# Optimization experiments

Measured on AMD Instinct MI355X. Metric: run time of the kernel, lower is better.

Reference implementation:

```python
import jax, jax.numpy as jnp
import numpy as np

N_NODES = 50000
N_EDGES = 800000
D_FEAT = 128
HIDDEN = 128
OUT = 64
HEADS = 4


def setup_inputs() -> dict:
    key = jax.random.key(0)
    ks = jax.random.split(key, 12)
    s_in = 1.0 / np.sqrt(D_FEAT)
    s_h = 1.0 / np.sqrt(HIDDEN)
    x = jax.random.normal(ks[0], (N_NODES, D_FEAT), dtype=jnp.float32)
    edge_index = jax.random.randint(ks[1], (2, N_EDGES), 0, N_NODES, dtype=jnp.int32)
    return {
        "x": x,
        "edge_index": edge_index,
        # SAGEConv params: lin_l (aggregated neighbors), lin_r (root), bias
        "W_l": jax.random.normal(ks[2], (D_FEAT, HIDDEN), dtype=jnp.float32) * s_in,
        "W_r": jax.random.normal(ks[3], (D_FEAT, HIDDEN), dtype=jnp.float32) * s_in,
        "b_sage": jnp.zeros((HIDDEN,), dtype=jnp.float32),
        # GATConv params: lin_src, lin_dst (heads*hidden each), att vectors, bias
        "W_src": jax.random.normal(ks[4], (HIDDEN, HEADS * HIDDEN), dtype=jnp.float32) * s_h,
        "W_dst": jax.random.normal(ks[5], (HIDDEN, HEADS * HIDDEN), dtype=jnp.float32) * s_h,
        "att_src": jax.random.normal(ks[6], (HEADS, HIDDEN), dtype=jnp.float32) * s_h,
        "att_dst": jax.random.normal(ks[7], (HEADS, HIDDEN), dtype=jnp.float32) * s_h,
        "b_gat": jnp.zeros((HIDDEN,), dtype=jnp.float32),
        # Final Linear
        "W_lin": jax.random.normal(ks[8], (HIDDEN, OUT), dtype=jnp.float32) * s_h,
        "b_lin": jnp.zeros((OUT,), dtype=jnp.float32),
    }


def reference(x, edge_index, W_l, W_r, b_sage, W_src, W_dst, att_src, att_dst, b_gat, W_lin, b_lin):
    N = x.shape[0]
    src = edge_index[0]
    dst = edge_index[1]

    # ---- SAGEConv (mean aggregation): out = lin_l(mean_j x_j) + lin_r(x_i) + b ----
    agg = jax.ops.segment_sum(x[src], dst, num_segments=N)          # [N, d]
    cnt = jax.ops.segment_sum(jnp.ones_like(dst, dtype=x.dtype), dst, num_segments=N)
    mean_nbr = agg / jnp.maximum(cnt, 1.0)[:, None]
    h = mean_nbr @ W_l + x @ W_r + b_sage                           # [N, H*... no: [N, hidden]
    h = jax.nn.relu(h)

    # ---- GATConv (heads=4, concat=False -> mean over heads) ----
    H, C = att_src.shape
    hs = (h @ W_src).reshape(N, H, C)                               # source-transformed [N, H, C]
    hd = (h @ W_dst).reshape(N, H, C)                               # dest-transformed   [N, H, C]
    a_s = jnp.einsum('nhc,hc->nh', hs, att_src)                     # [N, H]
    a_d = jnp.einsum('nhc,hc->nh', hd, att_dst)                     # [N, H]
    e = jax.nn.leaky_relu(a_s[src] + a_d[dst], negative_slope=0.2)  # [E, H]
    # edge softmax over incoming edges per destination node
    e_max = jax.ops.segment_max(e, dst, num_segments=N)             # [N, H]
    e_exp = jnp.exp(e - e_max[dst])                                 # [E, H]
    denom = jax.ops.segment_sum(e_exp, dst, num_segments=N)         # [N, H]
    alpha = e_exp / denom[dst]                                      # [E, H]
    msg = hs[src] * alpha[:, :, None]                               # [E, H, C]
    out = jax.ops.segment_sum(msg, dst, num_segments=N)             # [N, H, C]
    out = out.mean(axis=1) + b_gat                                  # concat=False: avg heads
    out = jax.nn.relu(out)

    # ---- final Linear ----
    return out @ W_lin + b_lin
```

## Files before the change

kernel.cpp:

```cpp
#include <hip/hip_runtime.h>

#define D 128
#define HEADS 4

typedef __attribute__((ext_vector_type(8))) short short8;
typedef __attribute__((ext_vector_type(4))) float f32x4;

static __device__ __forceinline__ float leaky(float v) { return v > 0.f ? v : 0.2f * v; }

static __device__ __forceinline__ float2 bf2_to_f2(unsigned int u) {
    float2 r;
    union { unsigned int i; float f; } a, b;
    a.i = (u & 0xffffu) << 16;
    b.i = u & 0xffff0000u;
    r.x = a.f; r.y = b.f;
    return r;
}
static __device__ __forceinline__ float bf_to_f(unsigned short s) {
    union { unsigned int i; float f; } a;
    a.i = ((unsigned int)s) << 16;
    return a.f;
}
static __device__ __forceinline__ unsigned short f2bf(float f) {
    union { float f; unsigned int i; } v; v.f = f;
    unsigned int u = v.i;
    unsigned int r = (u + 0x7fffu + ((u >> 16) & 1u)) >> 16;
    return (unsigned short)r;
}

#define CPAD 16
#define HIST_BLOCKS 128
#define PREP_CNT 107520

__global__ __launch_bounds__(256) void k_early(const float* __restrict__ x,
                                               const int* __restrict__ ei, int E, int npairs,
                                               const float* __restrict__ Wl, const float* __restrict__ Wr,
                                               const float* __restrict__ Wsrc, const float* __restrict__ Wlin,
                                               const float* __restrict__ Wdst,
                                               const float* __restrict__ atts, const float* __restrict__ attd,
                                               unsigned short* __restrict__ Bh,
                                               unsigned short* __restrict__ Bg,
                                               unsigned short* __restrict__ Bf,
                                               float* __restrict__ wsd,
                                               unsigned int* __restrict__ xb,
                                               int* __restrict__ bhist) {
    __shared__ int sh[512];
    int gb = blockIdx.x, t = threadIdx.x;
    if (gb < HIST_BLOCKS) {
        for (int i = t; i < 512; i += 256) sh[i] = 0;
        __syncthreads();
        for (int i = gb * 256 + t; i < E; i += HIST_BLOCKS * 256)
            atomicAdd(&sh[ei[E + i] >> 7], 1);
        __syncthreads();
        for (int i = t; i < 512; i += 256) if (sh[i]) atomicAdd(&bhist[i * CPAD], sh[i]);
        return;
    }
    int i = (gb - HIST_BLOCKS) * 256 + t;
    if (i < 32768) {
        int idx = i;
        int j = idx & 7, n16 = (idx >> 3) & 15, quad = (idx >> 7) & 3, rest = idx >> 9;
        int nc = rest & 7, kb = rest >> 3;
        int kk = kb * 32 + quad * 8 + j;
        int n = nc * 16 + n16;
        float v = (kk < 128) ? Wl[kk * 128 + n] : Wr[(kk - 128) * 128 + n];
        Bh[idx] = f2bf(v);
    } else if (i < 32768 + 65536) {
        int idx = i - 32768;
        int j = idx & 7, n16 = (idx >> 3) & 15, quad = (idx >> 7) & 3, rest = idx >> 9;
        int nc = rest & 7, kb = rest >> 3;
        int kk = kb * 32 + quad * 8 + j;
        int n = nc * 16 + n16;
        float v = Wsrc[(kk & 127) * 512 + (kk >> 7) * 128 + n];
        Bg[idx] = f2bf(v);
    } else if (i < 32768 + 65536 + 8192) {
        int idx = i - 98304;
        int j = idx & 7, n16 = (idx >> 3) & 15, quad = (idx >> 7) & 3, rest = idx >> 9;
        int nc = rest & 3, kb = rest >> 2;
        int kk = kb * 32 + quad * 8 + j;
        int n = nc * 16 + n16;
        Bf[idx] = f2bf(Wlin[kk * 64 + n]);
    } else if (i < PREP_CNT) {
        int tt = i - 106496;
        int k = tt >> 3, o = tt & 7;
        int hh = o & 3;
        const float* W = (o < 4) ? Wsrc : Wdst;
        const float* att = (o < 4) ? atts : attd;
        float acc = 0.f;
        for (int c = 0; c < 128; c++) acc += W[k * 512 + hh * 128 + c] * att[hh * 128 + c];
        wsd[k * 8 + o] = acc;
    } else {
        int p = i - PREP_CNT;
        if (p < npairs) {
            float2 v = *(const float2*)(x + (size_t)p * 2);
            xb[p] = (unsigned int)f2bf(v.x) | ((unsigned int)f2bf(v.y) << 16);
        }
    }
}

__global__ void k_bscan(const int* __restrict__ bhist, int nbuck, int E,
                        int* __restrict__ bbase, int* __restrict__ bcur,
                        int* __restrict__ rowptr, int N) {
    __shared__ int s[512];
    int t = threadIdx.x;
    int v = (t < nbuck) ? bhist[t * CPAD] : 0;
    s[t] = v;
    __syncthreads();
    for (int off = 1; off < 512; off <<= 1) {
        int tv = (t >= off) ? s[t - off] : 0;
        __syncthreads();
        s[t] += tv;
        __syncthreads();
    }
    if (t < nbuck) { int ex = s[t] - v; bbase[t] = ex; bcur[t * CPAD] = ex; }
    if (t == 0) { bbase[nbuck] = E; rowptr[N] = E; }
}

__global__ __launch_bounds__(256) void k_binscatter(const int* __restrict__ ei, int E,
                                                    int* __restrict__ bcur,
                                                    int2* __restrict__ ebuf) {
    int i = blockIdx.x * 256 + threadIdx.x;
    if (i < E) {
        int s = ei[i], d = ei[E + i];
        int pos = atomicAdd(&bcur[(d >> 7) * CPAD], 1);
        ebuf[pos] = make_int2(s, d);
    }
}

__global__ __launch_bounds__(256) void k_bucket_csr(const int2* __restrict__ ebuf,
                                                    const int* __restrict__ bbase,
                                                    int2* __restrict__ csr2,
                                                    int* __restrict__ rowptr, int N) {
    __shared__ int cnt[128];
    __shared__ int incl[128];
    __shared__ unsigned char off[4608];
    __shared__ int2 sorted[4608];
    int b = blockIdx.x;
    int e0 = bbase[b], e1 = bbase[b + 1];
    int ecnt = e1 - e0;
    if (ecnt > 4608) ecnt = 4608;
    int t = threadIdx.x;
    if (t < 128) cnt[t] = 0;
    __syncthreads();
    for (int i = t; i < ecnt; i += 256) {
        int d = ebuf[e0 + i].y & 127;
        off[i] = (unsigned char)atomicAdd(&cnt[d], 1);
    }
    __syncthreads();
    if (t < 128) incl[t] = cnt[t];
    __syncthreads();
    for (int o = 1; o < 128; o <<= 1) {
        int v = 0;
        if (t < 128 && t >= o) v = incl[t - o];
        __syncthreads();
        if (t < 128) incl[t] += v;
        __syncthreads();
    }
    int nbase0 = b << 7;
    if (t < 128) {
        int node = nbase0 + t;
        if (node < N) rowptr[node] = e0 + incl[t] - cnt[t];
    }
    __syncthreads();
    for (int i = t; i < ecnt; i += 256) {
        int2 e = ebuf[e0 + i];
        int d = e.y & 127;
        sorted[incl[d] - cnt[d] + off[i]] = e;
    }
    __syncthreads();
    for (int i = t; i < ecnt; i += 256) csr2[e0 + i] = sorted[i];
}

__global__ __launch_bounds__(256) void k_sage_mean(const int* __restrict__ rowptr,
                                                   const int2* __restrict__ csr2,
                                                   const unsigned int* __restrict__ xb,
                                                   unsigned int* __restrict__ meanb, int N) {
    int n = blockIdx.x * 4 + (threadIdx.x >> 6);
    if (n >= N) return;
    int lane = threadIdx.x & 63;
    int e0 = rowptr[n], e1 = rowptr[n + 1];
    float ax = 0.f, ay = 0.f;
    int e = e0;
    for (; e + 3 < e1; e += 4) {
        int s0 = csr2[e].x, s1 = csr2[e + 1].x, s2 = csr2[e + 2].x, s3 = csr2[e + 3].x;
        unsigned int u0 = xb[(size_t)s0 * 64 + lane];
        unsigned int u1 = xb[(size_t)s1 * 64 + lane];
        unsigned int u2 = xb[(size_t)s2 * 64 + lane];
        unsigned int u3 = xb[(size_t)s3 * 64 + lane];
        float2 v0 = bf2_to_f2(u0), v1 = bf2_to_f2(u1), v2 = bf2_to_f2(u2), v3 = bf2_to_f2(u3);
        ax += (v0.x + v1.x) + (v2.x + v3.x);
        ay += (v0.y + v1.y) + (v2.y + v3.y);
    }
    for (; e < e1; e++) {
        int s0 = csr2[e].x;
        float2 v0 = bf2_to_f2(xb[(size_t)s0 * 64 + lane]);
        ax += v0.x; ay += v0.y;
    }
    int dg = e1 - e0;
    float inv = 1.0f / (float)(dg > 0 ? dg : 1);
    unsigned int o = (unsigned int)f2bf(ax * inv) | ((unsigned int)f2bf(ay * inv) << 16);
    __builtin_nontemporal_store(o, meanb + (size_t)n * 64 + lane);
}

__global__ __launch_bounds__(256) void k_mfma_h(const unsigned short* __restrict__ A0,
                                                const unsigned short* __restrict__ A1,
                                                const unsigned short* __restrict__ Bp,
                                                const float* __restrict__ bias,
                                                const float* __restrict__ wsd,
                                                unsigned short* __restrict__ outb,
                                                float* __restrict__ a_s,
                                                float* __restrict__ a_d, int M) {
    const int NC = 8;
    __shared__ unsigned short sH[64][136];
    __shared__ float swsd[1024];
    int tid = threadIdx.x;
    int wave = tid >> 6;
    int lane = tid & 63;
    int row0 = blockIdx.x * 64 + wave * 16;
    int n16 = lane & 15, quad = lane >> 4;
    int arow = row0 + n16;
    int arowc = arow < M ? arow : 0;
    for (int i = tid; i < 1024; i += 256) swsd[i] = wsd[i];
    f32x4 acc[NC];
    #pragma unroll
    for (int i = 0; i < NC; i++) acc[i] = (f32x4){0.f, 0.f, 0.f, 0.f};
    #pragma unroll
    for (int kb = 0; kb < 8; kb++) {
        const unsigned short* ap = (kb < 4)
            ? (A0 + (size_t)arowc * 128 + kb * 32 + quad * 8)
            : (A1 + (size_t)arowc * 128 + (kb - 4) * 32 + quad * 8);
        short8 af = *(const short8*)ap;
        #pragma unroll
        for (int nc = 0; nc < NC; nc++) {
            short8 bf = *(const short8*)(Bp + ((((size_t)(kb * NC + nc) * 4 + quad) * 16 + n16) << 3));
            acc[nc] = __builtin_amdgcn_mfma_f32_16x16x32_bf16(af, bf, acc[nc], 0, 0, 0);
        }
    }
    int orow = row0 + quad * 4;
    int lrow = wave * 16 + quad * 4;
    #pragma unroll
    for (int r = 0; r < 4; r++) {
        int m = orow + r;
        #pragma unroll
        for (int nc = 0; nc < NC; nc++) {
            int col = nc * 16 + n16;
            float v = fmaxf(acc[nc][r] + bias[col], 0.f);
            unsigned short bv = f2bf(v);
            sH[lrow + r][col] = bv;
            if (m < M) outb[(size_t)m * 128 + col] = bv;
        }
    }
    __syncthreads();
    #pragma unroll
    for (int j = tid; j < 512; j += 256) {
        int m = j >> 3, o = j & 7;
        float accd = 0.f;
        #pragma unroll 4
        for (int k = 0; k < 128; k++)
            accd += bf_to_f(sH[m][k]) * swsd[k * 8 + o];
        int n = blockIdx.x * 64 + m;
        if (n < M) {
            if (o < 4) a_s[n * 4 + o] = accd;
            else       a_d[n * 4 + (o - 4)] = accd;
        }
    }
}

#define EDGE_CAP 192
__global__ __launch_bounds__(256) void k_gat_agg(const int* __restrict__ rowptr,
                                                 const int2* __restrict__ csr2,
                                                 const unsigned int* __restrict__ hb,
                                                 const float* __restrict__ a_s,
                                                 const float* __restrict__ a_d,
                                                 unsigned int* __restrict__ aggb, int N) {
    __shared__ int   sSrc[4][EDGE_CAP];
    __shared__ float sAl[4][EDGE_CAP * 4];
    int wv = threadIdx.x >> 6;
    int lane = threadIdx.x & 63;
    int n = blockIdx.x * 4 + wv;
    bool active = n < N;
    int e0 = 0, deg = 0;
    float4 ad = {0.f, 0.f, 0.f, 0.f};
    if (active) {
        e0 = rowptr[n];
        deg = rowptr[n + 1] - e0;
        ad = *(const float4*)(a_d + (size_t)n * 4);
    }
    f32x4 psum = {0.f, 0.f, 0.f, 0.f};
    for (int base = 0; base < deg; base += 64) {
        int i = base + lane;
        if (i < deg) {
            int s = csr2[e0 + i].x;
            float4 as = *(const float4*)(a_s + (size_t)s * 4);
            f32x4 w;
            w.x = __expf(leaky(as.x + ad.x));
            w.y = __expf(leaky(as.y + ad.y));
            w.z = __expf(leaky(as.z + ad.z));
            w.w = __expf(leaky(as.w + ad.w));
            psum += w;
            if (i < EDGE_CAP) {
                sSrc[wv][i] = s;
                *(f32x4*)&sAl[wv][i * 4] = w;
            }
        }
    }
    #pragma unroll
    for (int o = 32; o; o >>= 1) {
        psum.x += __shfl_xor(psum.x, o);
        psum.y += __shfl_xor(psum.y, o);
        psum.z += __shfl_xor(psum.z, o);
        psum.w += __shfl_xor(psum.w, o);
    }
    f32x4 inv;
    inv.x = psum.x > 0.f ? 0.25f / psum.x : 0.f;
    inv.y = psum.y > 0.f ? 0.25f / psum.y : 0.f;
    inv.z = psum.z > 0.f ? 0.25f / psum.z : 0.f;
    inv.w = psum.w > 0.f ? 0.25f / psum.w : 0.f;
    int capdeg = deg < EDGE_CAP ? deg : EDGE_CAP;
    for (int base = 0; base < capdeg; base += 64) {
        int i = base + lane;
        if (i < capdeg) {
            f32x4 w = *(f32x4*)&sAl[wv][i * 4];
            w *= inv;
            *(f32x4*)&sAl[wv][i * 4] = w;
        }
    }
    __syncthreads();
    float2 ac0 = {0, 0}, ac1 = {0, 0}, ac2 = {0, 0}, ac3 = {0, 0};
    int e = 0;
    for (; e + 3 < capdeg; e += 4) {
        int s0 = sSrc[wv][e], s1 = sSrc[wv][e + 1], s2 = sSrc[wv][e + 2], s3 = sSrc[wv][e + 3];
        f32x4 w0 = *(const f32x4*)&sAl[wv][e * 4];
        f32x4 w1 = *(const f32x4*)&sAl[wv][e * 4 + 4];
        f32x4 w2 = *(const f32x4*)&sAl[wv][e * 4 + 8];
        f32x4 w3 = *(const f32x4*)&sAl[wv][e * 4 + 12];
        unsigned int u0 = hb[(size_t)s0 * 64 + lane];
        unsigned int u1 = hb[(size_t)s1 * 64 + lane];
        unsigned int u2 = hb[(size_t)s2 * 64 + lane];
        unsigned int u3 = hb[(size_t)s3 * 64 + lane];
        float2 v0 = bf2_to_f2(u0), v1 = bf2_to_f2(u1), v2 = bf2_to_f2(u2), v3 = bf2_to_f2(u3);
        ac0.x += w0.x * v0.x + w1.x * v1.x + w2.x * v2.x + w3.x * v3.x;
        ac0.y += w0.x * v0.y + w1.x * v1.y + w2.x * v2.y + w3.x * v3.y;
        ac1.x += w0.y * v0.x + w1.y * v1.x + w2.y * v2.x + w3.y * v3.x;
        ac1.y += w0.y * v0.y + w1.y * v1.y + w2.y * v2.y + w3.y * v3.y;
        ac2.x += w0.z * v0.x + w1.z * v1.x + w2.z * v2.x + w3.z * v3.x;
        ac2.y += w0.z * v0.y + w1.z * v1.y + w2.z * v2.y + w3.z * v3.y;
        ac3.x += w0.w * v0.x + w1.w * v1.x + w2.w * v2.x + w3.w * v3.x;
        ac3.y += w0.w * v0.y + w1.w * v1.y + w2.w * v2.y + w3.w * v3.y;
    }
    for (; e < capdeg; e++) {
        int s0 = sSrc[wv][e];
        f32x4 w0 = *(const f32x4*)&sAl[wv][e * 4];
        unsigned int u0 = hb[(size_t)s0 * 64 + lane];
        float2 v0 = bf2_to_f2(u0);
        ac0.x += w0.x * v0.x; ac0.y += w0.x * v0.y;
        ac1.x += w0.y * v0.x; ac1.y += w0.y * v0.y;
        ac2.x += w0.z * v0.x; ac2.y += w0.z * v0.y;
        ac3.x += w0.w * v0.x; ac3.y += w0.w * v0.y;
    }
    for (int i = EDGE_CAP; i < deg; i++) {
        int s = csr2[e0 + i].x;
        float4 as = *(const float4*)(a_s + (size_t)s * 4);
        f32x4 w;
        w.x = __expf(leaky(as.x + ad.x)) * inv.x;
        w.y = __expf(leaky(as.y + ad.y)) * inv.y;
        w.z = __expf(leaky(as.z + ad.z)) * inv.z;
        w.w = __expf(leaky(as.w + ad.w)) * inv.w;
        float2 v0 = bf2_to_f2(hb[(size_t)s * 64 + lane]);
        ac0.x += w.x * v0.x; ac0.y += w.x * v0.y;
        ac1.x += w.y * v0.x; ac1.y += w.y * v0.y;
        ac2.x += w.z * v0.x; ac2.y += w.z * v0.y;
        ac3.x += w.w * v0.x; ac3.y += w.w * v0.y;
    }
    if (!active) return;
    unsigned int* rowu = aggb + (size_t)n * 256 + lane;
    unsigned int o0 = (unsigned int)f2bf(ac0.x) | ((unsigned int)f2bf(ac0.y) << 16);
    unsigned int o1 = (unsigned int)f2bf(ac1.x) | ((unsigned int)f2bf(ac1.y) << 16);
    unsigned int o2 = (unsigned int)f2bf(ac2.x) | ((unsigned int)f2bf(ac2.y) << 16);
    unsigned int o3 = (unsigned int)f2bf(ac3.x) | ((unsigned int)f2bf(ac3.y) << 16);
    __builtin_nontemporal_store(o0, rowu + 0);
    __builtin_nontemporal_store(o1, rowu + 64);
    __builtin_nontemporal_store(o2, rowu + 128);
    __builtin_nontemporal_store(o3, rowu + 192);
}

__global__ __launch_bounds__(256) void k_mfma_tail(const unsigned short* __restrict__ aggb,
                                                   const unsigned short* __restrict__ Bg,
                                                   const float* __restrict__ bg,
                                                   const unsigned short* __restrict__ Bf,
                                                   const float* __restrict__ bl,
                                                   float* __restrict__ out, int M) {
    __shared__ unsigned short sG[64][136];
    int wave = threadIdx.x >> 6;
    int lane = threadIdx.x & 63;
    int row0 = blockIdx.x * 64 + wave * 16;
    int n16 = lane & 15, quad = lane >> 4;
    {
        int arow = row0 + n16;
        int arowc = arow < M ? arow : 0;
        const unsigned short* ap = aggb + (size_t)arowc * 512 + quad * 8;
        f32x4 acc[8];
        #pragma unroll
        for (int i = 0; i < 8; i++) acc[i] = (f32x4){0.f, 0.f, 0.f, 0.f};
        #pragma unroll
        for (int kb = 0; kb < 16; kb++) {
            short8 af = *(const short8*)(ap + kb * 32);
            #pragma unroll
            for (int nc = 0; nc < 8; nc++) {
                short8 bf = *(const short8*)(Bg + ((((size_t)(kb * 8 + nc) * 4 + quad) * 16 + n16) << 3));
                acc[nc] = __builtin_amdgcn_mfma_f32_16x16x32_bf16(af, bf, acc[nc], 0, 0, 0);
            }
        }
        int lrow = wave * 16 + quad * 4;
        #pragma unroll
        for (int r = 0; r < 4; r++) {
            #pragma unroll
            for (int nc = 0; nc < 8; nc++) {
                int col = nc * 16 + n16;
                sG[lrow + r][col] = f2bf(fmaxf(acc[nc][r] + bg[col], 0.f));
            }
        }
    }
    __syncthreads();
    {
        f32x4 acc[4];
        #pragma unroll
        for (int i = 0; i < 4; i++) acc[i] = (f32x4){0.f, 0.f, 0.f, 0.f};
        #pragma unroll
        for (int kb = 0; kb < 4; kb++) {
            short8 af = *(const short8*)&sG[wave * 16 + n16][kb * 32 + quad * 8];
            #pragma unroll
            for (int nc = 0; nc < 4; nc++) {
                short8 bf = *(const short8*)(Bf + ((((size_t)(kb * 4 + nc) * 4 + quad) * 16 + n16) << 3));
                acc[nc] = __builtin_amdgcn_mfma_f32_16x16x32_bf16(af, bf, acc[nc], 0, 0, 0);
            }
        }
        int orow = row0 + quad * 4;
        #pragma unroll
        for (int r = 0; r < 4; r++) {
            int m = orow + r;
            if (m < M) {
                #pragma unroll
                for (int nc = 0; nc < 4; nc++) {
                    int col = nc * 16 + n16;
                    out[(size_t)m * 64 + col] = acc[nc][r] + bl[col];
                }
            }
        }
    }
}

extern "C" void kernel_launch(void* const* d_in, const int* in_sizes, int n_in,
                              void* d_out, int out_size, void* d_ws, size_t ws_size,
                              hipStream_t stream) {
    const float* x    = (const float*)d_in[0];
    const int*   ei   = (const int*)d_in[1];
    const float* Wl   = (const float*)d_in[2];
    const float* Wr   = (const float*)d_in[3];
    const float* bs   = (const float*)d_in[4];
    const float* Wsrc = (const float*)d_in[5];
    const float* Wdst = (const float*)d_in[6];
    const float* atts = (const float*)d_in[7];
    const float* attd = (const float*)d_in[8];
    const float* bg   = (const float*)d_in[9];
    const float* Wlin = (const float*)d_in[10];
    const float* bl   = (const float*)d_in[11];
    int N = in_sizes[0] / D;
    int E = in_sizes[1] / 2;
    int nbuck = (N + 127) >> 7;
    int npairs = N * 64;

    char* w = (char*)d_ws;
    auto alloc = [&](size_t bytes) {
        char* p = w;
        w += (bytes + 255) & ~(size_t)255;
        return p;
    };
    unsigned int* xb     = (unsigned int*)alloc((size_t)N * 256);
    unsigned int* meanb  = (unsigned int*)alloc((size_t)N * 256);
    unsigned int* hb     = (unsigned int*)alloc((size_t)N * 256);
    unsigned int* aggb   = (unsigned int*)alloc((size_t)N * 1024);
    unsigned short* Bh   = (unsigned short*)alloc(65536 * 2);
    unsigned short* Bg   = (unsigned short*)alloc(65536 * 2);
    unsigned short* Bf   = (unsigned short*)alloc(8192 * 2);
    float* a_s           = (float*)alloc((size_t)N * 16);
    float* a_d           = (float*)alloc((size_t)N * 16);
    float* wsd           = (float*)alloc(1024 * 4);
    int* rowptr          = (int*)alloc((size_t)(N + 512) * 4);
    int* bhist           = (int*)alloc(512 * CPAD * 4);
    int* bbase           = (int*)alloc(513 * 4);
    int* bcur            = (int*)alloc(512 * CPAD * 4);
    int2* ebuf           = (int2*)alloc((size_t)E * 8);
    int2* csr2           = (int2*)alloc((size_t)E * 8);
    (void)ws_size; (void)n_in; (void)out_size;

    hipMemsetAsync(bhist, 0, 512 * CPAD * 4, stream);

    int workBlocks = (PREP_CNT + npairs + 255) / 256;
    k_early<<<HIST_BLOCKS + workBlocks, 256, 0, stream>>>(x, ei, E, npairs,
                                                          Wl, Wr, Wsrc, Wlin, Wdst, atts, attd,
                                                          Bh, Bg, Bf, wsd, xb, bhist);
    k_bscan<<<1, 512, 0, stream>>>(bhist, nbuck, E, bbase, bcur, rowptr, N);
    k_binscatter<<<(E + 255) / 256, 256, 0, stream>>>(ei, E, bcur, ebuf);
    k_bucket_csr<<<nbuck, 256, 0, stream>>>(ebuf, bbase, csr2, rowptr, N);

    k_sage_mean<<<(N + 3) / 4, 256, 0, stream>>>(rowptr, csr2, xb, meanb, N);
    k_mfma_h<<<(N + 63) / 64, 256, 0, stream>>>((const unsigned short*)meanb,
                                                (const unsigned short*)xb, Bh, bs, wsd,
                                                (unsigned short*)hb, a_s, a_d, N);
    k_gat_agg<<<(N + 3) / 4, 256, 0, stream>>>(rowptr, csr2, hb, a_s, a_d, aggb, N);
    k_mfma_tail<<<(N + 63) / 64, 256, 0, stream>>>((const unsigned short*)aggb, Bg, bg,
                                                   Bf, bl, (float*)d_out, N);
}
```

Measured before the change: 294.4 us.

## Fuse CSR bucket sort with SAGE mean aggregation using 32-node buckets

Shrinks destination buckets from 128 to 32 nodes and packs each edge into one 32-bit word (16-bit source plus 5-bit local destination). A new kernel sorts each bucket in shared memory and immediately computes the SAGE neighbour means from the sorted sources, replacing the separate CSR-build and mean kernels. The CSR also drops from int2 to int, which halves edge-index traffic in the GAT aggregation. The trade-offs are that the 16-bit packing only holds for fewer than 65536 nodes, each bucket is capped at 1024 edges, and each wave now processes 8 nodes serially.

```diff
diff --git a/kernel.cpp b/kernel.cpp
--- a/kernel.cpp
+++ b/kernel.cpp
@@ -31,6 +31,7 @@
 #define CPAD 16
 #define HIST_BLOCKS 128
 #define PREP_CNT 107520
+#define MAXBUCK 2048
 
 __global__ __launch_bounds__(256) void k_early(const float* __restrict__ x,
                                                const int* __restrict__ ei, int E, int npairs,
@@ -44,15 +45,15 @@
                                                float* __restrict__ wsd,
                                                unsigned int* __restrict__ xb,
                                                int* __restrict__ bhist) {
-    __shared__ int sh[512];
+    __shared__ int sh[MAXBUCK];
     int gb = blockIdx.x, t = threadIdx.x;
     if (gb < HIST_BLOCKS) {
-        for (int i = t; i < 512; i += 256) sh[i] = 0;
+        for (int i = t; i < MAXBUCK; i += 256) sh[i] = 0;
         __syncthreads();
         for (int i = gb * 256 + t; i < E; i += HIST_BLOCKS * 256)
-            atomicAdd(&sh[ei[E + i] >> 7], 1);
+            atomicAdd(&sh[ei[E + i] >> 5], 1);
         __syncthreads();
-        for (int i = t; i < 512; i += 256) if (sh[i]) atomicAdd(&bhist[i * CPAD], sh[i]);
+        for (int i = t; i < MAXBUCK; i += 256) if (sh[i]) atomicAdd(&bhist[i * CPAD], sh[i]);
         return;
     }
     int i = (gb - HIST_BLOCKS) * 256 + t;
@@ -97,108 +98,115 @@
     }
 }
 
-__global__ void k_bscan(const int* __restrict__ bhist, int nbuck, int E,
-                        int* __restrict__ bbase, int* __restrict__ bcur,
-                        int* __restrict__ rowptr, int N) {
-    __shared__ int s[512];
+__global__ __launch_bounds__(256) void k_bscan(const int* __restrict__ bhist, int nbuck, int E,
+                                               int* __restrict__ bbase, int* __restrict__ bcur,
+                                               int* __restrict__ rowptr, int N) {
+    __shared__ int ssum[256];
     int t = threadIdx.x;
-    int v = (t < nbuck) ? bhist[t * CPAD] : 0;
-    s[t] = v;
-    __syncthreads();
-    for (int off = 1; off < 512; off <<= 1) {
-        int tv = (t >= off) ? s[t - off] : 0;
+    int base = t * 8;
+    int v[8]; int s = 0;
+    #pragma unroll
+    for (int j = 0; j < 8; j++) {
+        int idx = base + j;
+        v[j] = (idx < nbuck) ? bhist[idx * CPAD] : 0;
+        s += v[j];
+    }
+    ssum[t] = s;
+    __syncthreads();
+    for (int o = 1; o < 256; o <<= 1) {
+        int tv = (t >= o) ? ssum[t - o] : 0;
         __syncthreads();
-        s[t] += tv;
+        ssum[t] += tv;
         __syncthreads();
     }
-    if (t < nbuck) { int ex = s[t] - v; bbase[t] = ex; bcur[t * CPAD] = ex; }
+    int run = ssum[t] - s;
+    #pragma unroll
+    for (int j = 0; j < 8; j++) {
+        int idx = base + j;
+        if (idx < nbuck) { bbase[idx] = run; bcur[idx * CPAD] = run; }
+        run += v[j];
+    }
     if (t == 0) { bbase[nbuck] = E; rowptr[N] = E; }
 }
 
 __global__ __launch_bounds__(256) void k_binscatter(const int* __restrict__ ei, int E,
                                                     int* __restrict__ bcur,
-                                                    int2* __restrict__ ebuf) {
+                                                    unsigned int* __restrict__ ebuf) {
     int i = blockIdx.x * 256 + threadIdx.x;
     if (i < E) {
         int s = ei[i], d = ei[E + i];
-        int pos = atomicAdd(&bcur[(d >> 7) * CPAD], 1);
-        ebuf[pos] = make_int2(s, d);
-    }
-}
-
-__global__ __launch_bounds__(256) void k_bucket_csr(const int2* __restrict__ ebuf,
+        int pos = atomicAdd(&bcur[(d >> 5) * CPAD], 1);
+        ebuf[pos] = (unsigned int)s | ((unsigned int)(d & 31) << 16);
+    }
+}
+
+#define BCAP 1024
+__global__ __launch_bounds__(256) void k_build_sage(const unsigned int* __restrict__ ebuf,
                                                     const int* __restrict__ bbase,
-                                                    int2* __restrict__ csr2,
-                                                    int* __restrict__ rowptr, int N) {
-    __shared__ int cnt[128];
-    __shared__ int incl[128];
-    __shared__ unsigned char off[4608];
-    __shared__ int2 sorted[4608];
-    int b = blockIdx.x;
+                                                    const unsigned int* __restrict__ xb,
+                                                    int* __restrict__ csr,
+                                                    int* __restrict__ rowptr,
+                                                    unsigned int* __restrict__ meanb, int N) {
+    __shared__ int cnt[32];
+    __shared__ int excl[33];
+    __shared__ unsigned char off[BCAP];
+    __shared__ unsigned int rawv[BCAP];
+    __shared__ int sorted[BCAP];
+    int b = blockIdx.x, t = threadIdx.x;
     int e0 = bbase[b], e1 = bbase[b + 1];
     int ecnt = e1 - e0;
-    if (ecnt > 4608) ecnt = 4608;
-    int t = threadIdx.x;
-    if (t < 128) cnt[t] = 0;
+    if (ecnt > BCAP) ecnt = BCAP;
+    if (t < 32) cnt[t] = 0;
     __syncthreads();
     for (int i = t; i < ecnt; i += 256) {
-        int d = ebuf[e0 + i].y & 127;
-        off[i] = (unsigned char)atomicAdd(&cnt[d], 1);
-    }
-    __syncthreads();
-    if (t < 128) incl[t] = cnt[t];
-    __syncthreads();
-    for (int o = 1; o < 128; o <<= 1) {
-        int v = 0;
-        if (t < 128 && t >= o) v = incl[t - o];
-        __syncthreads();
-        if (t < 128) incl[t] += v;
-        __syncthreads();
-    }
-    int nbase0 = b << 7;
-    if (t < 128) {
-        int node = nbase0 + t;
-        if (node < N) rowptr[node] = e0 + incl[t] - cnt[t];
+        unsigned int p = ebuf[e0 + i];
+        rawv[i] = p;
+        off[i] = (unsigned char)atomicAdd(&cnt[(p >> 16) & 31], 1);
+    }
+    __syncthreads();
+    if (t == 0) {
+        int run = 0;
+        #pragma unroll
+        for (int j = 0; j < 32; j++) { excl[j] = run; run += cnt[j]; }
+        excl[32] = run;
     }
     __syncthreads();
     for (int i = t; i < ecnt; i += 256) {
-        int2 e = ebuf[e0 + i];
-        int d = e.y & 127;
-        sorted[incl[d] - cnt[d] + off[i]] = e;
-    }
-    __syncthreads();
-    for (int i = t; i < ecnt; i += 256) csr2[e0 + i] = sorted[i];
-}
-
-__global__ __launch_bounds__(256) void k_sage_mean(const int* __restrict__ rowptr,
-                                                   const int2* __restrict__ csr2,
-                                                   const unsigned int* __restrict__ xb,
-                                                   unsigned int* __restrict__ meanb, int N) {
-    int n = blockIdx.x * 4 + (threadIdx.x >> 6);
-    if (n >= N) return;
-    int lane = threadIdx.x & 63;
-    int e0 = rowptr[n], e1 = rowptr[n + 1];
-    float ax = 0.f, ay = 0.f;
-    int e = e0;
-    for (; e + 3 < e1; e += 4) {
-        int s0 = csr2[e].x, s1 = csr2[e + 1].x, s2 = csr2[e + 2].x, s3 = csr2[e + 3].x;
-        unsigned int u0 = xb[(size_t)s0 * 64 + lane];
-        unsigned int u1 = xb[(size_t)s1 * 64 + lane];
-        unsigned int u2 = xb[(size_t)s2 * 64 + lane];
-        unsigned int u3 = xb[(size_t)s3 * 64 + lane];
-        float2 v0 = bf2_to_f2(u0), v1 = bf2_to_f2(u1), v2 = bf2_to_f2(u2), v3 = bf2_to_f2(u3);
-        ax += (v0.x + v1.x) + (v2.x + v3.x);
-        ay += (v0.y + v1.y) + (v2.y + v3.y);
-    }
-    for (; e < e1; e++) {
-        int s0 = csr2[e].x;
-        float2 v0 = bf2_to_f2(xb[(size_t)s0 * 64 + lane]);
-        ax += v0.x; ay += v0.y;
-    }
-    int dg = e1 - e0;
-    float inv = 1.0f / (float)(dg > 0 ? dg : 1);
-    unsigned int o = (unsigned int)f2bf(ax * inv) | ((unsigned int)f2bf(ay * inv) << 16);
-    __builtin_nontemporal_store(o, meanb + (size_t)n * 64 + lane);
+        unsigned int p = rawv[i];
+        int d = (p >> 16) & 31;
+        sorted[excl[d] + off[i]] = (int)(p & 0xffffu);
+    }
+    __syncthreads();
+    int nb0 = b << 5;
+    if (t < 32 && nb0 + t < N) rowptr[nb0 + t] = e0 + excl[t];
+    for (int i = t; i < ecnt; i += 256) csr[e0 + i] = sorted[i];
+    int wv = t >> 6, lane = t & 63;
+    for (int k = 0; k < 8; k++) {
+        int local = wv * 8 + k;
+        int node = nb0 + local;
+        if (node >= N) continue;
+        int le0 = excl[local], le1 = excl[local + 1];
+        float ax = 0.f, ay = 0.f;
+        int e = le0;
+        for (; e + 3 < le1; e += 4) {
+            int s0 = sorted[e], s1 = sorted[e + 1], s2 = sorted[e + 2], s3 = sorted[e + 3];
+            unsigned int u0 = xb[(size_t)s0 * 64 + lane];
+            unsigned int u1 = xb[(size_t)s1 * 64 + lane];
+            unsigned int u2 = xb[(size_t)s2 * 64 + lane];
+            unsigned int u3 = xb[(size_t)s3 * 64 + lane];
+            float2 v0 = bf2_to_f2(u0), v1 = bf2_to_f2(u1), v2 = bf2_to_f2(u2), v3 = bf2_to_f2(u3);
+            ax += (v0.x + v1.x) + (v2.x + v3.x);
+            ay += (v0.y + v1.y) + (v2.y + v3.y);
+        }
+        for (; e < le1; e++) {
+            float2 v0 = bf2_to_f2(xb[(size_t)sorted[e] * 64 + lane]);
+            ax += v0.x; ay += v0.y;
+        }
+        int dg = le1 - le0;
+        float inv = 1.0f / (float)(dg > 0 ? dg : 1);
+        unsigned int o = (unsigned int)f2bf(ax * inv) | ((unsigned int)f2bf(ay * inv) << 16);
+        __builtin_nontemporal_store(o, meanb + (size_t)node * 64 + lane);
+    }
 }
 
 __global__ __launch_bounds__(256) void k_mfma_h(const unsigned short* __restrict__ A0,
@@ -267,7 +275,7 @@
 
 #define EDGE_CAP 192
 __global__ __launch_bounds__(256) void k_gat_agg(const int* __restrict__ rowptr,
-                                                 const int2* __restrict__ csr2,
+                                                 const int* __restrict__ csr,
                                                  const unsigned int* __restrict__ hb,
                                                  const float* __restrict__ a_s,
                                                  const float* __restrict__ a_d,
@@ -289,7 +297,7 @@
     for (int base = 0; base < deg; base += 64) {
         int i = base + lane;
         if (i < deg) {
-            int s = csr2[e0 + i].x;
+            int s = csr[e0 + i];
             float4 as = *(const float4*)(a_s + (size_t)s * 4);
             f32x4 w;
             w.x = __expf(leaky(as.x + ad.x));
@@ -358,7 +366,7 @@
         ac3.x += w0.w * v0.x; ac3.y += w0.w * v0.y;
     }
     for (int i = EDGE_CAP; i < deg; i++) {
-        int s = csr2[e0 + i].x;
+        int s = csr[e0 + i];
         float4 as = *(const float4*)(a_s + (size_t)s * 4);
         f32x4 w;
         w.x = __expf(leaky(as.x + ad.x)) * inv.x;
@@ -466,7 +474,7 @@
     const float* bl   = (const float*)d_in[11];
     int N = in_sizes[0] / D;
     int E = in_sizes[1] / 2;
-    int nbuck = (N + 127) >> 7;
+    int nbuck = (N + 31) >> 5;
     int npairs = N * 64;
 
     char* w = (char*)d_ws;
@@ -485,29 +493,28 @@
     float* a_s           = (float*)alloc((size_t)N * 16);
     float* a_d           = (float*)alloc((size_t)N * 16);
     float* wsd           = (float*)alloc(1024 * 4);
-    int* rowptr          = (int*)alloc((size_t)(N + 512) * 4);
-    int* bhist           = (int*)alloc(512 * CPAD * 4);
-    int* bbase           = (int*)alloc(513 * 4);
-    int* bcur            = (int*)alloc(512 * CPAD * 4);
-    int2* ebuf           = (int2*)alloc((size_t)E * 8);
-    int2* csr2           = (int2*)alloc((size_t)E * 8);
+    int* rowptr          = (int*)alloc((size_t)(N + 64) * 4);
+    int* bhist           = (int*)alloc((size_t)MAXBUCK * CPAD * 4);
+    int* bbase           = (int*)alloc((size_t)(MAXBUCK + 1) * 4);
+    int* bcur            = (int*)alloc((size_t)MAXBUCK * CPAD * 4);
+    unsigned int* ebuf   = (unsigned int*)alloc((size_t)E * 4);
+    int* csr             = (int*)alloc((size_t)E * 4);
     (void)ws_size; (void)n_in; (void)out_size;
 
-    hipMemsetAsync(bhist, 0, 512 * CPAD * 4, stream);
+    hipMemsetAsync(bhist, 0, (size_t)MAXBUCK * CPAD * 4, stream);
 
     int workBlocks = (PREP_CNT + npairs + 255) / 256;
     k_early<<<HIST_BLOCKS + workBlocks, 256, 0, stream>>>(x, ei, E, npairs,
                                                           Wl, Wr, Wsrc, Wlin, Wdst, atts, attd,
                                                           Bh, Bg, Bf, wsd, xb, bhist);
-    k_bscan<<<1, 512, 0, stream>>>(bhist, nbuck, E, bbase, bcur, rowptr, N);
+    k_bscan<<<1, 256, 0, stream>>>(bhist, nbuck, E, bbase, bcur, rowptr, N);
     k_binscatter<<<(E + 255) / 256, 256, 0, stream>>>(ei, E, bcur, ebuf);
-    k_bucket_csr<<<nbuck, 256, 0, stream>>>(ebuf, bbase, csr2, rowptr, N);
-
-    k_sage_mean<<<(N + 3) / 4, 256, 0, stream>>>(rowptr, csr2, xb, meanb, N);
+    k_build_sage<<<nbuck, 256, 0, stream>>>(ebuf, bbase, xb, csr, rowptr, meanb, N);
+
     k_mfma_h<<<(N + 63) / 64, 256, 0, stream>>>((const unsigned short*)meanb,
                                                 (const unsigned short*)xb, Bh, bs, wsd,
                                                 (unsigned short*)hb, a_s, a_d, N);
-    k_gat_agg<<<(N + 3) / 4, 256, 0, stream>>>(rowptr, csr2, hb, a_s, a_d, aggb, N);
+    k_gat_agg<<<(N + 3) / 4, 256, 0, stream>>>(rowptr, csr, hb, a_s, a_d, aggb, N);
     k_mfma_tail<<<(N + 63) / 64, 256, 0, stream>>>((const unsigned short*)aggb, Bg, bg,
                                                    Bf, bl, (float*)d_out, N);
 }
```

Result: faster. 287.6 us (-2.3%).
